# Kernel tuning notes

Hardware: AMD Instinct MI355X
Metric: run time of the kernel (lower is better)

Reference implementation:

```python
import jax, jax.numpy as jnp
import numpy as np

N, E, G = 20000, 320000, 64
H, NF, EF, L, Z = 280, 5, 4, 3, 64
BN_EPS = 1e-5


def _bn(x, g, b):
    # BatchNorm1d in training mode: batch stats over dim 0, biased variance
    m = x.mean(0)
    v = x.var(0)
    return g * (x - m) * jax.lax.rsqrt(v + BN_EPS) + b


def _mlp(x, W1, b1, g1, be1, W2, b2, g2, be2):
    h = jax.nn.relu(_bn(x @ W1 + b1, g1, be1))
    return jax.nn.relu(_bn(h @ W2 + b2, g2, be2))


def setup_inputs() -> dict:
    key = jax.random.key(0)
    ks = jax.random.split(key, 24)
    s = 0.05
    inp = {
        "x": jax.random.normal(ks[0], (N, NF), jnp.float32),
        "edge_attr": jax.random.normal(ks[1], (E, EF), jnp.float32),
        "edge_index": jax.random.randint(ks[2], (2, E), 0, N),
        "batch": jnp.sort(jax.random.randint(ks[3], (N,), 0, G)),
        # input layer
        "Wi": jax.random.normal(ks[4], (NF, H), jnp.float32) * s,
        "bi": jnp.zeros((H,), jnp.float32),
        # message MLP (stacked over L layers): in = 2H+EF
        "Wm1": jax.random.normal(ks[5], (L, 2 * H + EF, H), jnp.float32) * s,
        "bm1": jnp.zeros((L, H), jnp.float32),
        "g1": jnp.ones((L, H), jnp.float32),
        "be1": jnp.zeros((L, H), jnp.float32),
        "Wm2": jax.random.normal(ks[6], (L, H, H), jnp.float32) * s,
        "bm2": jnp.zeros((L, H), jnp.float32),
        "g2": jnp.ones((L, H), jnp.float32),
        "be2": jnp.zeros((L, H), jnp.float32),
        # update MLP: in = 2H
        "Wu1": jax.random.normal(ks[7], (L, 2 * H, H), jnp.float32) * s,
        "bu1": jnp.zeros((L, H), jnp.float32),
        "g3": jnp.ones((L, H), jnp.float32),
        "be3": jnp.zeros((L, H), jnp.float32),
        "Wu2": jax.random.normal(ks[8], (L, H, H), jnp.float32) * s,
        "bu2": jnp.zeros((L, H), jnp.float32),
        "g4": jnp.ones((L, H), jnp.float32),
        "be4": jnp.zeros((L, H), jnp.float32),
        # mu head
        "Wmu": jax.random.normal(ks[9], (H, Z), jnp.float32) * s,
        "bmu": jnp.zeros((Z,), jnp.float32),
    }
    return inp


def reference(x, edge_attr, Wi, bi, Wm1, bm1, g1, be1, Wm2, bm2, g2, be2,
              Wu1, bu1, g3, be3, Wu2, bu2, g4, be4, Wmu, bmu,
              edge_index, batch):
    src, dst = edge_index[0], edge_index[1]
    h = x @ Wi + bi  # [N, H]
    for l in range(L):
        # message: cat(h_i=h[dst], h_j=h[src], edge_attr) -> MLP -> [E, H]
        msg_in = jnp.concatenate([h[dst], h[src], edge_attr], axis=-1)
        msg = _mlp(msg_in, Wm1[l], bm1[l], g1[l], be1[l], Wm2[l], bm2[l], g2[l], be2[l])
        # aggregate: scatter-add into target nodes
        agg = jax.ops.segment_sum(msg, dst, num_segments=N)
        # update: cat(h, agg) -> MLP; residual in GNNEncoder
        upd = _mlp(jnp.concatenate([h, agg], axis=-1),
                   Wu1[l], bu1[l], g3[l], be3[l], Wu2[l], bu2[l], g4[l], be4[l])
        h = h + upd
    # global mean pool over graphs
    sums = jax.ops.segment_sum(h, batch, num_segments=G)
    cnt = jax.ops.segment_sum(jnp.ones((h.shape[0],), h.dtype), batch, num_segments=G)
    pooled = sums / jnp.maximum(cnt, 1.0)[:, None]
    return pooled @ Wmu + bmu  # [G, Z]
```

## Files before the change

### kernel.cpp

```cpp
#include <hip/hip_runtime.h>
#include <hip/hip_bf16.h>

#define NN 20000
#define EE 320000
#define GG 64
#define HH 280
#define NFF 5
#define EFF 4
#define LL 3
#define ZZ 64
#define BN_EPS 1e-5f

typedef __hip_bfloat16 bf;
typedef unsigned short ush;
typedef __attribute__((ext_vector_type(8))) short v8s;
typedef __attribute__((ext_vector_type(4))) float v4f;

__device__ __forceinline__ float us2f(ush u) {
  return __uint_as_float(((unsigned)u) << 16);
}
__device__ __forceinline__ ush f2us(float v) {
  bf b = __float2bfloat16(v);
  return *reinterpret_cast<ush*>(&b);
}
__device__ __forceinline__ int clampi(int v, int hi) {
  return v < 0 ? 0 : (v >= hi ? hi - 1 : v);
}

__global__ void probe_k(const void* __restrict__ x, int* __restrict__ flag) {
  __shared__ int sh[256];
  int tid = threadIdx.x;
  int cnt = 0;
  for (int i = tid; i < 2048; i += 256) {
    ush w = ((const ush*)x)[i];
    unsigned e = (w >> 7) & 0xFF;
    if (w != 0 && (e < 87 || e > 167)) cnt++;
  }
  sh[tid] = cnt;
  __syncthreads();
  for (int o = 128; o > 0; o >>= 1) {
    if (tid < o) sh[tid] += sh[tid + o];
    __syncthreads();
  }
  if (tid == 0) *flag = (sh[0] > 64) ? 1 : 0;
}

__global__ void convert_k(const void* __restrict__ src, float* __restrict__ dst,
                          int n, const int* __restrict__ flag) {
  int i = blockIdx.x * 256 + threadIdx.x;
  if (i < n) {
    if (*flag)
      dst[i] = ((const float*)src)[i];
    else
      dst[i] = us2f(((const ush*)src)[i]);
  }
}

__global__ void wt_ab_k(const float* __restrict__ W, ush* __restrict__ O) {
  int i = blockIdx.x * 256 + threadIdx.x;
  if (i >= 3 * 576 * 288) return;
  int l = i / 165888, r = i % 165888;
  int n = r / 288, k = r % 288;
  float v = 0.f;
  if (n < 560 && k < 280)
    v = (n < 280) ? W[(size_t)l * 157920 + (size_t)k * 280 + n]
                  : W[(size_t)l * 157920 + (size_t)(280 + k) * 280 + (n - 280)];
  O[i] = f2us(v);
}
__global__ void wt_sq_k(const float* __restrict__ W, ush* __restrict__ O) {
  int i = blockIdx.x * 256 + threadIdx.x;
  if (i >= 3 * 320 * 288) return;
  int l = i / 92160, r = i % 92160;
  int n = r / 288, k = r % 288;
  float v = (n < 280 && k < 280) ? W[(size_t)l * 78400 + (size_t)k * 280 + n] : 0.f;
  O[i] = f2us(v);
}
__global__ void wt_u1_k(const float* __restrict__ W, ush* __restrict__ O) {
  int i = blockIdx.x * 256 + threadIdx.x;
  if (i >= 3 * 320 * 576) return;
  int l = i / 184320, r = i % 184320;
  int n = r / 576, k = r % 576;
  float v = (n < 280 && k < 560) ? W[(size_t)l * 156800 + (size_t)k * 280 + n] : 0.f;
  O[i] = f2us(v);
}

struct MG {
  const ush* A;
  const ush* Bt;
  const float* bias;
  void* C;
  float* stats;
  int M, K, Nn, lda, ldb, ldc;
};

template <int CB, int ST>
__global__ __launch_bounds__(256) void mgemm_k(MG g) {
  __shared__ ush Bs[64][296];
  auto red = (float(*)[64])Bs;
  int t = threadIdx.x;
  int n0 = blockIdx.x * 64, m0 = blockIdx.y * 128;
  int lane = t & 63, wv = t >> 6;
  int lrow = lane & 15, quad = lane >> 4;
  int br = t >> 2;
  int bc = (t & 3) * 72;
  v4f acc[2][4];
#pragma unroll
  for (int gi = 0; gi < 2; ++gi)
#pragma unroll
    for (int ci = 0; ci < 4; ++ci) acc[gi][ci] = (v4f){0.f, 0.f, 0.f, 0.f};

  const ush* Arow[2];
  bool av[2];
#pragma unroll
  for (int gi = 0; gi < 2; ++gi) {
    int gm = m0 + (wv << 5) + (gi << 4) + lrow;
    av[gi] = gm < g.M;
    Arow[gi] = g.A + (size_t)gm * g.lda + (quad << 3);
  }
  const ush* Brow = g.Bt + (size_t)(n0 + br) * g.ldb + bc;
  uint4 zz = {0, 0, 0, 0};

  int ntile = g.K / 288;
  for (int tile = 0; tile < ntile; ++tile) {
    int k0 = tile * 288;
    uint4 aR[2][9];
#pragma unroll
    for (int kt = 0; kt < 9; ++kt)
#pragma unroll
      for (int gi = 0; gi < 2; ++gi)
        aR[gi][kt] =
            av[gi] ? *(const uint4*)(Arow[gi] + k0 + (kt << 5)) : zz;
    if (tile) __syncthreads();
#pragma unroll
    for (int i = 0; i < 9; ++i)
      *(uint4*)&Bs[br][bc + (i << 3)] = *(const uint4*)(Brow + k0 + (i << 3));
    __syncthreads();
#pragma unroll
    for (int kt = 0; kt < 9; ++kt) {
      v8s bq[4];
#pragma unroll
      for (int ci = 0; ci < 4; ++ci)
        bq[ci] = *(const v8s*)&Bs[(ci << 4) + lrow][(kt << 5) + (quad << 3)];
#pragma unroll
      for (int gi = 0; gi < 2; ++gi) {
        v8s af = *(v8s*)&aR[gi][kt];
#pragma unroll
        for (int ci = 0; ci < 4; ++ci)
          acc[gi][ci] = __builtin_amdgcn_mfma_f32_16x16x32_bf16(
              af, bq[ci], acc[gi][ci], 0, 0, 0);
      }
    }
  }

  float bj[4];
#pragma unroll
  for (int ci = 0; ci < 4; ++ci) {
    int gn = n0 + (ci << 4) + lrow;
    bj[ci] = (g.bias && gn < g.Nn) ? g.bias[gn] : 0.f;
  }
#pragma unroll
  for (int gi = 0; gi < 2; ++gi)
#pragma unroll
    for (int ci = 0; ci < 4; ++ci)
#pragma unroll
      for (int r = 0; r < 4; ++r) {
        int gm = m0 + (wv << 5) + (gi << 4) + (quad << 2) + r;
        int gn = n0 + (ci << 4) + lrow;
        float v = acc[gi][ci][r] + bj[ci];
        bool ok = (gm < g.M) && (gn < g.Nn);
        if (ok) {
          size_t idx = (size_t)gm * g.ldc + gn;
          if (CB)
            ((ush*)g.C)[idx] = f2us(v);
          else
            ((float*)g.C)[idx] = v;
        }
        acc[gi][ci][r] = ok ? v : 0.f;
      }
  if (ST) {
    int rowg = (wv << 2) | quad;
    __syncthreads();
#pragma unroll
    for (int ci = 0; ci < 4; ++ci) {
      float s = 0.f;
#pragma unroll
      for (int gi = 0; gi < 2; ++gi)
#pragma unroll
        for (int r = 0; r < 4; ++r) s += acc[gi][ci][r];
      red[rowg][(ci << 4) | lrow] = s;
    }
    __syncthreads();
    if (t < 64) {
      float s = 0.f;
#pragma unroll
      for (int r = 0; r < 16; ++r) s += red[r][t];
      int gn = n0 + t;
      if (gn < g.Nn) atomicAdd(&g.stats[gn], s);
    }
    __syncthreads();
#pragma unroll
    for (int ci = 0; ci < 4; ++ci) {
      float s = 0.f;
#pragma unroll
      for (int gi = 0; gi < 2; ++gi)
#pragma unroll
        for (int r = 0; r < 4; ++r) s += acc[gi][ci][r] * acc[gi][ci][r];
      red[rowg][(ci << 4) | lrow] = s;
    }
    __syncthreads();
    if (t < 64) {
      float s = 0.f;
#pragma unroll
      for (int r = 0; r < 16; ++r) s += red[r][t];
      int gn = n0 + t;
      if (gn < g.Nn) atomicAdd(&g.stats[HH + gn], s);
    }
  }
}

__global__ __launch_bounds__(256) void gemm_small_k(
    const float* __restrict__ A, const float* __restrict__ B,
    const float* __restrict__ bias, void* __restrict__ C,
    const int* __restrict__ flag, int M, int K, int Nn, int lda, int ldb,
    int ldc, int outmode) {
  __shared__ alignas(16) float As[16][68];
  __shared__ alignas(16) float Bsm[16][68];
  int tid = threadIdx.x;
  int n0 = blockIdx.x * 64, m0 = blockIdx.y * 64;
  int tx = tid & 15, ty = tid >> 4;
  int am = tid >> 2, akq = (tid & 3) << 2;
  int bk = tid >> 4, bn = (tid & 15) << 2;
  float acc[4][4] = {};
  int gmA = m0 + am;
  int nkt = (K + 15) >> 4;
  for (int kt = 0; kt < nkt; ++kt) {
    int k0 = kt << 4;
#pragma unroll
    for (int i = 0; i < 4; ++i) {
      int gk = k0 + akq + i;
      As[akq + i][am] = (gmA < M && gk < K) ? A[(size_t)gmA * lda + gk] : 0.f;
    }
    {
      int gk = k0 + bk;
      bool kin = gk < K;
#pragma unroll
      for (int j = 0; j < 4; ++j) {
        int gn = n0 + bn + j;
        Bsm[bk][bn + j] = (kin && gn < Nn) ? B[(size_t)gk * ldb + gn] : 0.f;
      }
    }
    __syncthreads();
#pragma unroll
    for (int kk = 0; kk < 16; ++kk) {
      float4 a4 = *(const float4*)&As[kk][ty << 2];
      float4 b4 = *(const float4*)&Bsm[kk][tx << 2];
      float av[4] = {a4.x, a4.y, a4.z, a4.w};
      float bv[4] = {b4.x, b4.y, b4.z, b4.w};
#pragma unroll
      for (int i = 0; i < 4; ++i)
#pragma unroll
        for (int j = 0; j < 4; ++j) acc[i][j] = fmaf(av[i], bv[j], acc[i][j]);
    }
    __syncthreads();
  }
  int ofl = outmode ? *flag : -1;
#pragma unroll
  for (int i = 0; i < 4; ++i) {
    int gm = m0 + (ty << 2) + i;
    if (gm < M) {
#pragma unroll
      for (int j = 0; j < 4; ++j) {
        int gn = n0 + (tx << 2) + j;
        if (gn < Nn) {
          float v = acc[i][j] + (bias ? bias[gn] : 0.f);
          size_t idx = (size_t)gm * ldc + gn;
          if (outmode == 0)
            ((float*)C)[idx] = v;
          else if (ofl)
            ((float*)C)[idx] = v;
          else
            ((ush*)C)[idx] = f2us(v);
        }
      }
    }
  }
}

__global__ __launch_bounds__(256) void edge_stats_k(
    const int* __restrict__ eids, const int* __restrict__ dst,
    const int* __restrict__ src, const float* __restrict__ ea,
    const ush* __restrict__ Pq, const float* __restrict__ W1c,
    const float* __restrict__ b1, float* __restrict__ stats) {
  __shared__ int dstl[256], srcl[256];
  __shared__ float4 eal[256];
  __shared__ float w1cs[4 * HH];
  __shared__ float b1s[HH];
  int tid = threadIdx.x;
  int e0 = blockIdx.x * 256;
  {
    int e = clampi(eids[e0 + tid], EE);
    dstl[tid] = clampi(dst[e], NN);
    srcl[tid] = clampi(src[e], NN);
    eal[tid] = *(const float4*)(ea + (size_t)e * 4);
  }
  for (int i = tid; i < 4 * HH; i += 256) w1cs[i] = W1c[i];
  for (int i = tid; i < HH; i += 256) b1s[i] = b1[i];
  __syncthreads();
  int c0 = tid, c1 = tid + 256;
  bool has1 = c1 < HH;
  float s0 = 0.f, q0 = 0.f, s1 = 0.f, q1 = 0.f;
  for (int e = 0; e < 256; ++e) {
    int d = dstl[e], sn = srcl[e];
    float4 ev = eal[e];
    {
      float raw = us2f(Pq[(size_t)d * 576 + c0]) + us2f(Pq[(size_t)sn * 576 + 280 + c0]);
      float r = ev.x * w1cs[c0] + ev.y * w1cs[HH + c0] +
                ev.z * w1cs[2 * HH + c0] + ev.w * w1cs[3 * HH + c0];
      float tv = raw + r + b1s[c0];
      s0 += tv; q0 += tv * tv;
    }
    if (has1) {
      float raw = us2f(Pq[(size_t)d * 576 + c1]) + us2f(Pq[(size_t)sn * 576 + 280 + c1]);
      float r = ev.x * w1cs[c1] + ev.y * w1cs[HH + c1] +
                ev.z * w1cs[2 * HH + c1] + ev.w * w1cs[3 * HH + c1];
      float tv = raw + r + b1s[c1];
      s1 += tv; q1 += tv * tv;
    }
  }
  atomicAdd(&stats[c0], s0);
  atomicAdd(&stats[HH + c0], q0);
  if (has1) {
    atomicAdd(&stats[c1], s1);
    atomicAdd(&stats[HH + c1], q1);
  }
}

__global__ void bn_finalize_k(const float* __restrict__ stats, float cnt,
                              const float* __restrict__ gw,
                              const float* __restrict__ bw,
                              const float* __restrict__ extra,
                              float* __restrict__ scale,
                              float* __restrict__ shift) {
  int c = threadIdx.x;
  if (c < HH) {
    float m = stats[c] / cnt;
    float v = stats[HH + c] / cnt - m * m;
    v = v < 0.f ? 0.f : v;
    float r = rsqrtf(v + BN_EPS);
    float sc = gw[c] * r;
    float sh = bw[c] - sc * m + (extra ? sc * extra[c] : 0.f);
    scale[c] = sc;
    shift[c] = sh;
  }
}

__global__ void hist_k(const int* __restrict__ dst, int* __restrict__ counts) {
  int e = blockIdx.x * 256 + threadIdx.x;
  if (e < EE) atomicAdd(&counts[clampi(dst[e], NN)], 1);
}

__global__ __launch_bounds__(1024) void scan_k(const int* __restrict__ counts,
                                               int* __restrict__ offs, int n) {
  __shared__ int buf[1024];
  __shared__ int running;
  int tid = threadIdx.x;
  if (tid == 0) running = 0;
  __syncthreads();
  for (int base = 0; base < n; base += 1024) {
    int v = (base + tid < n) ? counts[base + tid] : 0;
    buf[tid] = v;
    __syncthreads();
    for (int off = 1; off < 1024; off <<= 1) {
      int t = (tid >= off) ? buf[tid - off] : 0;
      __syncthreads();
      buf[tid] += t;
      __syncthreads();
    }
    int incl = buf[tid];
    if (base + tid < n) offs[base + tid] = running + incl - v;
    __syncthreads();
    if (tid == 1023) running += incl;
    __syncthreads();
  }
  if (tid == 0) offs[n] = running;
}

__global__ void fill_k(const int* __restrict__ dst, const int* __restrict__ offs,
                       int* __restrict__ cursor, int* __restrict__ eids) {
  int e = blockIdx.x * 256 + threadIdx.x;
  if (e < EE) {
    int n = clampi(dst[e], NN);
    int pos = atomicAdd(&cursor[n], 1);
    int idx = offs[n] + pos;
    if (idx >= 0 && idx < EE) eids[idx] = e;
  }
}

__global__ __launch_bounds__(256) void build_t1_k(
    const int* __restrict__ eids, const int* __restrict__ dst,
    const int* __restrict__ src, const float* __restrict__ ea,
    const ush* __restrict__ Pq, const float* __restrict__ W1c,
    const float* __restrict__ sc, const float* __restrict__ sh,
    ush* __restrict__ T1, int cb) {
  __shared__ float scs[HH], shs[HH], w1[4 * HH];
  int t = threadIdx.x;
  for (int i = t; i < HH; i += 256) { scs[i] = sc[i]; shs[i] = sh[i]; }
  for (int i = t; i < 4 * HH; i += 256) w1[i] = W1c[i];
  __syncthreads();
  int base = blockIdx.x * 32;
  int c2 = t + 256;
  bool h2 = c2 < HH;
  for (int i = 0; i < 32; ++i) {
    int r = cb + base + i;
    int e = clampi(eids[r], EE);
    int d = clampi(dst[e], NN), s = clampi(src[e], NN);
    float4 ev = *(const float4*)(ea + (size_t)e * 4);
    size_t pd = (size_t)d * 576, ps = (size_t)s * 576 + 280;
    size_t orow = (size_t)(base + i) * 288;
    {
      int c = t;
      float v = us2f(Pq[pd + c]) + us2f(Pq[ps + c]) + ev.x * w1[c] +
                ev.y * w1[HH + c] + ev.z * w1[2 * HH + c] + ev.w * w1[3 * HH + c];
      v = fmaf(scs[c], v, shs[c]);
      T1[orow + c] = f2us(v > 0.f ? v : 0.f);
    }
    if (h2) {
      int c = c2;
      float v = us2f(Pq[pd + c]) + us2f(Pq[ps + c]) + ev.x * w1[c] +
                ev.y * w1[HH + c] + ev.z * w1[2 * HH + c] + ev.w * w1[3 * HH + c];
      v = fmaf(scs[c], v, shs[c]);
      T1[orow + c] = f2us(v > 0.f ? v : 0.f);
    }
  }
}

__global__ __launch_bounds__(256) void aggregate_k(
    const int* __restrict__ offs, const ush* __restrict__ tmp2,
    const float* __restrict__ scale, const float* __restrict__ shift,
    float* __restrict__ agg, int e0, int e1) {
  int n = blockIdx.x;
  int rs = offs[n], re = offs[n + 1];
  if (rs < e0) rs = e0;
  if (re > e1) re = e1;
  if (rs >= re) return;
  int t = threadIdx.x;
  int c2 = t + 256;
  bool h2 = c2 < HH;
  float a0 = 0.f, a1 = 0.f;
  float sc0 = scale[t], sh0 = shift[t];
  float sc1 = h2 ? scale[c2] : 0.f, sh1 = h2 ? shift[c2] : 0.f;
  for (int r = rs; r < re; ++r) {
    const ush* row = tmp2 + (size_t)(r - e0) * HH;
    float v0 = fmaf(sc0, us2f(row[t]), sh0);
    a0 += v0 > 0.f ? v0 : 0.f;
    if (h2) {
      float v1 = fmaf(sc1, us2f(row[c2]), sh1);
      a1 += v1 > 0.f ? v1 : 0.f;
    }
  }
  agg[(size_t)n * HH + t] += a0;
  if (h2) agg[(size_t)n * HH + c2] += a1;
}

__global__ void hb_k(const float* __restrict__ h, ush* __restrict__ hcat) {
  int i = blockIdx.x * 256 + threadIdx.x;
  if (i < NN * HH) {
    int n = i / HH, c = i % HH;
    hcat[(size_t)n * 576 + c] = f2us(h[i]);
  }
}
__global__ void agg2hcat_k(const float* __restrict__ agg, ush* __restrict__ hcat) {
  int i = blockIdx.x * 256 + threadIdx.x;
  if (i < NN * HH) {
    int n = i / HH, c = i % HH;
    hcat[(size_t)n * 576 + 280 + c] = f2us(agg[i]);
  }
}
__global__ void u2a_k(const float* __restrict__ u1, const float* __restrict__ sc,
                      const float* __restrict__ sh, ush* __restrict__ u2A) {
  int i = blockIdx.x * 256 + threadIdx.x;
  if (i < NN * HH) {
    int n = i / HH, c = i % HH;
    float v = fmaf(sc[c], u1[i], sh[c]);
    u2A[(size_t)n * 288 + c] = f2us(v > 0.f ? v : 0.f);
  }
}
__global__ void residual_k(float* __restrict__ h, const float* __restrict__ u2,
                           const float* __restrict__ scale,
                           const float* __restrict__ shift) {
  int i = blockIdx.x * 256 + threadIdx.x;
  if (i < NN * HH) {
    int c = i % HH;
    float v = fmaf(scale[c], u2[i], shift[c]);
    h[i] += v > 0.f ? v : 0.f;
  }
}

__device__ __forceinline__ int lowerb(const int* a, int n, int key) {
  int lo = 0, hi = n;
  while (lo < hi) {
    int mid = (lo + hi) >> 1;
    if (a[mid] < key) lo = mid + 1; else hi = mid;
  }
  return lo;
}

__global__ __launch_bounds__(256) void pool_k(const float* __restrict__ h,
                                              const int* __restrict__ batch,
                                              float* __restrict__ pooled) {
  __shared__ float red[4][56];
  int gid = blockIdx.x, cc = blockIdx.y;
  int start = lowerb(batch, NN, gid);
  int end = lowerb(batch, NN, gid + 1);
  int cnt = end - start;
  float inv = 1.f / (float)(cnt > 1 ? cnt : 1);
  int grp = threadIdx.x >> 6, ci = threadIdx.x & 63;
  if (ci < 56) {
    int col = cc * 56 + ci;
    float s = 0.f;
    for (int n = start + grp; n < end; n += 4) s += h[(size_t)n * HH + col];
    red[grp][ci] = s;
  }
  __syncthreads();
  if (threadIdx.x < 56) {
    float s = red[0][threadIdx.x] + red[1][threadIdx.x] +
              red[2][threadIdx.x] + red[3][threadIdx.x];
    pooled[(size_t)gid * HH + cc * 56 + threadIdx.x] = s * inv;
  }
}

extern "C" void kernel_launch(void* const* d_in, const int* in_sizes, int n_in,
                              void* d_out, int out_size, void* d_ws,
                              size_t ws_size, hipStream_t stream) {
  const int* eidx = (const int*)d_in[2];
  const int* batch = (const int*)d_in[3];
  const int* srcp = eidx;
  const int* dstp = eidx + EE;
  size_t NH = (size_t)NN * HH;

  float* w0 = (float*)d_ws;
  size_t off = 0;
  auto alloc = [&](size_t n) {
    float* p = w0 + off;
    off += (n + 3) & ~(size_t)3;
    return p;
  };
  int* flag = (int*)alloc(4);
  float* cx = alloc(100000);
  float* cea = alloc(1280000);
  float* cWi = alloc(1400);
  float* cbi = alloc(280);
  float* cWm1 = alloc(473760);
  float* cbm1 = alloc(840);
  float* cg1 = alloc(840);
  float* cbe1 = alloc(840);
  float* cWm2 = alloc(235200);
  float* cbm2 = alloc(840);
  float* cg2 = alloc(840);
  float* cbe2 = alloc(840);
  float* cWu1 = alloc(470400);
  float* cbu1 = alloc(840);
  float* cg3 = alloc(840);
  float* cbe3 = alloc(840);
  float* cWu2 = alloc(235200);
  float* cbu2 = alloc(840);
  float* cg4 = alloc(840);
  float* cbe4 = alloc(840);
  float* cWmu = alloc(17920);
  float* cbmu = alloc(64);
  ush* W1ab = (ush*)alloc(248832);
  ush* W2t = (ush*)alloc(138240);
  ush* WU1t = (ush*)alloc(276480);
  ush* WU2t = (ush*)alloc(138240);
  float* h = alloc(NH);
  ush* hcat = (ush*)alloc(5824512);
  ush* u2A = hcat;
  float* pqr = alloc(5824512);
  ush* Pq = (ush*)pqr;
  float* u1f = pqr;
  float* agg = alloc(NH);
  float* pooled = alloc((size_t)GG * HH);
  float* stats = alloc(8 * HH);
  float* ss = alloc(8 * HH);
  int* counts = (int*)alloc(NN);
  int* offs = (int*)alloc(NN + 1);
  int* cursor = (int*)alloc(NN);
  int* eids = (int*)alloc(EE);
  size_t baseB = off * 4;

  int EC = 6400, T2 = 6400;
  {
    const int ecs[5] = {64000, 64000, 32000, 12800, 6400};
    const int t2s[5] = {EE, 64000, 32000, 12800, 6400};
    for (int i = 0; i < 5; ++i) {
      size_t need = baseB + (size_t)ecs[i] * 288 * 2 + (size_t)t2s[i] * 280 * 2 + 64;
      if (need <= ws_size) { EC = ecs[i]; T2 = t2s[i]; break; }
    }
  }
  ush* T1c = (ush*)(w0 + off);
  ush* tmp2 = T1c + (size_t)EC * 288;
  bool stored = (T2 == EE);
  int nch = EE / EC;

  probe_k<<<1, 256, 0, stream>>>(d_in[0], flag);
  struct Cv { const void* s; float* d; int n; };
  const Cv cv[22] = {
      {d_in[0], cx, NN * NFF},     {d_in[1], cea, EE * EFF},
      {d_in[4], cWi, NFF * HH},    {d_in[5], cbi, HH},
      {d_in[6], cWm1, LL * (2 * HH + EFF) * HH}, {d_in[7], cbm1, LL * HH},
      {d_in[8], cg1, LL * HH},     {d_in[9], cbe1, LL * HH},
      {d_in[10], cWm2, LL * HH * HH}, {d_in[11], cbm2, LL * HH},
      {d_in[12], cg2, LL * HH},    {d_in[13], cbe2, LL * HH},
      {d_in[14], cWu1, LL * 2 * HH * HH}, {d_in[15], cbu1, LL * HH},
      {d_in[16], cg3, LL * HH},    {d_in[17], cbe3, LL * HH},
      {d_in[18], cWu2, LL * HH * HH}, {d_in[19], cbu2, LL * HH},
      {d_in[20], cg4, LL * HH},    {d_in[21], cbe4, LL * HH},
      {d_in[22], cWmu, HH * ZZ},   {d_in[23], cbmu, ZZ}};
  for (int i = 0; i < 22; ++i)
    convert_k<<<(cv[i].n + 255) / 256, 256, 0, stream>>>(cv[i].s, cv[i].d, cv[i].n, flag);

  wt_ab_k<<<(3 * 576 * 288 + 255) / 256, 256, 0, stream>>>(cWm1, W1ab);
  wt_sq_k<<<(3 * 320 * 288 + 255) / 256, 256, 0, stream>>>(cWm2, W2t);
  wt_u1_k<<<(3 * 320 * 576 + 255) / 256, 256, 0, stream>>>(cWu1, WU1t);
  wt_sq_k<<<(3 * 320 * 288 + 255) / 256, 256, 0, stream>>>(cWu2, WU2t);

  gemm_small_k<<<dim3(5, 313), 256, 0, stream>>>(cx, cWi, cbi, h, nullptr, NN,
                                                 NFF, HH, NFF, HH, HH, 0);
  hipMemsetAsync(counts, 0, NN * sizeof(int), stream);
  hipMemsetAsync(cursor, 0, NN * sizeof(int), stream);
  hist_k<<<(EE + 255) / 256, 256, 0, stream>>>(dstp, counts);
  scan_k<<<1, 1024, 0, stream>>>(counts, offs, NN);
  fill_k<<<(EE + 255) / 256, 256, 0, stream>>>(dstp, offs, cursor, eids);

  int elemGrid = (int)((NH + 255) / 256);
  for (int l = 0; l < LL; ++l) {
    ush* Wab = W1ab + (size_t)l * 576 * 288;
    ush* W2l = W2t + (size_t)l * 320 * 288;
    ush* WU1l = WU1t + (size_t)l * 320 * 576;
    ush* WU2l = WU2t + (size_t)l * 320 * 288;
    const float* W1c = cWm1 + (size_t)l * 157920 + (size_t)560 * 280;
    float* st1 = stats; float* st2 = stats + 560;
    float* st3 = stats + 1120; float* st4 = stats + 1680;
    float* ss1 = ss; float* ss2 = ss + 560;
    float* ss3 = ss + 1120; float* ss4 = ss + 1680;
    hipMemsetAsync(stats, 0, 8 * HH * sizeof(float), stream);

    hb_k<<<elemGrid, 256, 0, stream>>>(h, hcat);
    {
      MG g = {hcat, Wab, nullptr, Pq, nullptr, NN, 288, 560, 576, 288, 576};
      mgemm_k<1, 0><<<dim3(9, 157), 256, 0, stream>>>(g);
    }
    edge_stats_k<<<EE / 256, 256, 0, stream>>>(eids, dstp, srcp, cea, Pq, W1c,
                                               cbm1 + l * HH, st1);
    bn_finalize_k<<<1, 320, 0, stream>>>(st1, (float)EE, cg1 + l * HH,
                                         cbe1 + l * HH, cbm1 + l * HH, ss1, ss1 + HH);
    for (int c = 0; c < nch; ++c) {
      int cb = c * EC;
      build_t1_k<<<EC / 32, 256, 0, stream>>>(eids, dstp, srcp, cea, Pq, W1c,
                                              ss1, ss1 + HH, T1c, cb);
      MG g = {T1c, W2l, cbm2 + l * HH,
              stored ? (void*)(tmp2 + (size_t)cb * HH) : (void*)tmp2, st2,
              EC, 288, HH, 288, 288, HH};
      mgemm_k<1, 1><<<dim3(5, EC / 128), 256, 0, stream>>>(g);
    }
    bn_finalize_k<<<1, 320, 0, stream>>>(st2, (float)EE, cg2 + l * HH,
                                         cbe2 + l * HH, nullptr, ss2, ss2 + HH);
    hipMemsetAsync(agg, 0, NH * sizeof(float), stream);
    if (stored) {
      aggregate_k<<<NN, 256, 0, stream>>>(offs, tmp2, ss2, ss2 + HH, agg, 0, EE);
    } else {
      for (int c = 0; c < nch; ++c) {
        int cb = c * EC;
        build_t1_k<<<EC / 32, 256, 0, stream>>>(eids, dstp, srcp, cea, Pq, W1c,
                                                ss1, ss1 + HH, T1c, cb);
        MG g = {T1c, W2l, cbm2 + l * HH, (void*)tmp2, nullptr,
                EC, 288, HH, 288, 288, HH};
        mgemm_k<1, 0><<<dim3(5, EC / 128), 256, 0, stream>>>(g);
        aggregate_k<<<NN, 256, 0, stream>>>(offs, tmp2, ss2, ss2 + HH, agg, cb, cb + EC);
      }
    }
    agg2hcat_k<<<elemGrid, 256, 0, stream>>>(agg, hcat);
    {
      MG g = {hcat, WU1l, cbu1 + l * HH, u1f, st3, NN, 576, HH, 576, 576, HH};
      mgemm_k<0, 1><<<dim3(5, 157), 256, 0, stream>>>(g);
    }
    bn_finalize_k<<<1, 320, 0, stream>>>(st3, (float)NN, cg3 + l * HH,
                                         cbe3 + l * HH, nullptr, ss3, ss3 + HH);
    u2a_k<<<elemGrid, 256, 0, stream>>>(u1f, ss3, ss3 + HH, u2A);
    {
      MG g = {u2A, WU2t + (size_t)l * 320 * 288, cbu2 + l * HH, agg, st4,
              NN, 288, HH, 288, 288, HH};
      mgemm_k<0, 1><<<dim3(5, 157), 256, 0, stream>>>(g);
    }
    bn_finalize_k<<<1, 320, 0, stream>>>(st4, (float)NN, cg4 + l * HH,
                                         cbe4 + l * HH, nullptr, ss4, ss4 + HH);
    residual_k<<<elemGrid, 256, 0, stream>>>(h, agg, ss4, ss4 + HH);
  }

  pool_k<<<dim3(GG, 5), 256, 0, stream>>>(h, batch, pooled);
  gemm_small_k<<<dim3(1, 1), 256, 0, stream>>>(pooled, cWmu, cbmu, d_out, flag,
                                               GG, HH, ZZ, HH, ZZ, ZZ, 1);
}
```

Measured before the change: 4.275 ms.

## Double GEMM M-tile to 256 rows and stream A fragments with rolling prefetch

Each wave now computes 64 rows instead of 32, so every B fragment read from shared memory feeds twice as many MFMAs and the B tile is loaded half as often overall. The A operand is no longer held in registers for the whole K tile; it is streamed through a 3-deep rotating register buffer that prefetches two K steps ahead. All launch grids are halved in the M dimension to match. The cost is more accumulator registers and fewer blocks, which can hurt occupancy and parallelism, especially for the 20000-row node GEMMs.

```diff
diff --git a/kernel.cpp b/kernel.cpp
--- a/kernel.cpp
+++ b/kernel.cpp
@@ -98,24 +98,24 @@
   __shared__ ush Bs[64][296];
   auto red = (float(*)[64])Bs;
   int t = threadIdx.x;
-  int n0 = blockIdx.x * 64, m0 = blockIdx.y * 128;
+  int n0 = blockIdx.x * 64, m0 = blockIdx.y * 256;
   int lane = t & 63, wv = t >> 6;
   int lrow = lane & 15, quad = lane >> 4;
   int br = t >> 2;
   int bc = (t & 3) * 72;
-  v4f acc[2][4];
-#pragma unroll
-  for (int gi = 0; gi < 2; ++gi)
-#pragma unroll
-    for (int ci = 0; ci < 4; ++ci) acc[gi][ci] = (v4f){0.f, 0.f, 0.f, 0.f};
-
-  const ush* Arow[2];
-  bool av[2];
-#pragma unroll
-  for (int gi = 0; gi < 2; ++gi) {
-    int gm = m0 + (wv << 5) + (gi << 4) + lrow;
-    av[gi] = gm < g.M;
-    Arow[gi] = g.A + (size_t)gm * g.lda + (quad << 3);
+  v4f acc[4][4];
+#pragma unroll
+  for (int mi = 0; mi < 4; ++mi)
+#pragma unroll
+    for (int ci = 0; ci < 4; ++ci) acc[mi][ci] = (v4f){0.f, 0.f, 0.f, 0.f};
+
+  const ush* Arow[4];
+  bool av[4];
+#pragma unroll
+  for (int mi = 0; mi < 4; ++mi) {
+    int gm = m0 + (wv << 6) + (mi << 4) + lrow;
+    av[mi] = gm < g.M;
+    Arow[mi] = g.A + (size_t)gm * g.lda + (quad << 3);
   }
   const ush* Brow = g.Bt + (size_t)(n0 + br) * g.ldb + bc;
   uint4 zz = {0, 0, 0, 0};
@@ -123,31 +123,36 @@
   int ntile = g.K / 288;
   for (int tile = 0; tile < ntile; ++tile) {
     int k0 = tile * 288;
-    uint4 aR[2][9];
-#pragma unroll
-    for (int kt = 0; kt < 9; ++kt)
-#pragma unroll
-      for (int gi = 0; gi < 2; ++gi)
-        aR[gi][kt] =
-            av[gi] ? *(const uint4*)(Arow[gi] + k0 + (kt << 5)) : zz;
     if (tile) __syncthreads();
 #pragma unroll
     for (int i = 0; i < 9; ++i)
       *(uint4*)&Bs[br][bc + (i << 3)] = *(const uint4*)(Brow + k0 + (i << 3));
+    uint4 ap[3][4];
+#pragma unroll
+    for (int mi = 0; mi < 4; ++mi) {
+      ap[0][mi] = av[mi] ? *(const uint4*)(Arow[mi] + k0) : zz;
+      ap[1][mi] = av[mi] ? *(const uint4*)(Arow[mi] + k0 + 32) : zz;
+    }
     __syncthreads();
 #pragma unroll
     for (int kt = 0; kt < 9; ++kt) {
+      if (kt + 2 < 9) {
+        int kn = k0 + ((kt + 2) << 5);
+#pragma unroll
+        for (int mi = 0; mi < 4; ++mi)
+          ap[(kt + 2) % 3][mi] = av[mi] ? *(const uint4*)(Arow[mi] + kn) : zz;
+      }
       v8s bq[4];
 #pragma unroll
       for (int ci = 0; ci < 4; ++ci)
         bq[ci] = *(const v8s*)&Bs[(ci << 4) + lrow][(kt << 5) + (quad << 3)];
 #pragma unroll
-      for (int gi = 0; gi < 2; ++gi) {
-        v8s af = *(v8s*)&aR[gi][kt];
+      for (int mi = 0; mi < 4; ++mi) {
+        v8s af = *(v8s*)&ap[kt % 3][mi];
 #pragma unroll
         for (int ci = 0; ci < 4; ++ci)
-          acc[gi][ci] = __builtin_amdgcn_mfma_f32_16x16x32_bf16(
-              af, bq[ci], acc[gi][ci], 0, 0, 0);
+          acc[mi][ci] = __builtin_amdgcn_mfma_f32_16x16x32_bf16(
+              af, bq[ci], acc[mi][ci], 0, 0, 0);
       }
     }
   }
@@ -159,14 +164,14 @@
     bj[ci] = (g.bias && gn < g.Nn) ? g.bias[gn] : 0.f;
   }
 #pragma unroll
-  for (int gi = 0; gi < 2; ++gi)
+  for (int mi = 0; mi < 4; ++mi)
 #pragma unroll
     for (int ci = 0; ci < 4; ++ci)
 #pragma unroll
       for (int r = 0; r < 4; ++r) {
-        int gm = m0 + (wv << 5) + (gi << 4) + (quad << 2) + r;
+        int gm = m0 + (wv << 6) + (mi << 4) + (quad << 2) + r;
         int gn = n0 + (ci << 4) + lrow;
-        float v = acc[gi][ci][r] + bj[ci];
+        float v = acc[mi][ci][r] + bj[ci];
         bool ok = (gm < g.M) && (gn < g.Nn);
         if (ok) {
           size_t idx = (size_t)gm * g.ldc + gn;
@@ -175,7 +180,7 @@
           else
             ((float*)g.C)[idx] = v;
         }
-        acc[gi][ci][r] = ok ? v : 0.f;
+        acc[mi][ci][r] = ok ? v : 0.f;
       }
   if (ST) {
     int rowg = (wv << 2) | quad;
@@ -184,9 +189,9 @@
     for (int ci = 0; ci < 4; ++ci) {
       float s = 0.f;
 #pragma unroll
-      for (int gi = 0; gi < 2; ++gi)
-#pragma unroll
-        for (int r = 0; r < 4; ++r) s += acc[gi][ci][r];
+      for (int mi = 0; mi < 4; ++mi)
+#pragma unroll
+        for (int r = 0; r < 4; ++r) s += acc[mi][ci][r];
       red[rowg][(ci << 4) | lrow] = s;
     }
     __syncthreads();
@@ -202,9 +207,9 @@
     for (int ci = 0; ci < 4; ++ci) {
       float s = 0.f;
 #pragma unroll
-      for (int gi = 0; gi < 2; ++gi)
-#pragma unroll
-        for (int r = 0; r < 4; ++r) s += acc[gi][ci][r] * acc[gi][ci][r];
+      for (int mi = 0; mi < 4; ++mi)
+#pragma unroll
+        for (int r = 0; r < 4; ++r) s += acc[mi][ci][r] * acc[mi][ci][r];
       red[rowg][(ci << 4) | lrow] = s;
     }
     __syncthreads();
@@ -648,7 +653,7 @@
     hb_k<<<elemGrid, 256, 0, stream>>>(h, hcat);
     {
       MG g = {hcat, Wab, nullptr, Pq, nullptr, NN, 288, 560, 576, 288, 576};
-      mgemm_k<1, 0><<<dim3(9, 157), 256, 0, stream>>>(g);
+      mgemm_k<1, 0><<<dim3(9, 79), 256, 0, stream>>>(g);
     }
     edge_stats_k<<<EE / 256, 256, 0, stream>>>(eids, dstp, srcp, cea, Pq, W1c,
                                                cbm1 + l * HH, st1);
@@ -661,7 +666,7 @@
       MG g = {T1c, W2l, cbm2 + l * HH,
               stored ? (void*)(tmp2 + (size_t)cb * HH) : (void*)tmp2, st2,
               EC, 288, HH, 288, 288, HH};
-      mgemm_k<1, 1><<<dim3(5, EC / 128), 256, 0, stream>>>(g);
+      mgemm_k<1, 1><<<dim3(5, EC / 256), 256, 0, stream>>>(g);
     }
     bn_finalize_k<<<1, 320, 0, stream>>>(st2, (float)EE, cg2 + l * HH,
                                          cbe2 + l * HH, nullptr, ss2, ss2 + HH);
@@ -675,22 +680,21 @@
                                                 ss1, ss1 + HH, T1c, cb);
         MG g = {T1c, W2l, cbm2 + l * HH, (void*)tmp2, nullptr,
                 EC, 288, HH, 288, 288, HH};
-        mgemm_k<1, 0><<<dim3(5, EC / 128), 256, 0, stream>>>(g);
+        mgemm_k<1, 0><<<dim3(5, EC / 256), 256, 0, stream>>>(g);
         aggregate_k<<<NN, 256, 0, stream>>>(offs, tmp2, ss2, ss2 + HH, agg, cb, cb + EC);
       }
     }
     agg2hcat_k<<<elemGrid, 256, 0, stream>>>(agg, hcat);
     {
       MG g = {hcat, WU1l, cbu1 + l * HH, u1f, st3, NN, 576, HH, 576, 576, HH};
-      mgemm_k<0, 1><<<dim3(5, 157), 256, 0, stream>>>(g);
+      mgemm_k<0, 1><<<dim3(5, 79), 256, 0, stream>>>(g);
     }
     bn_finalize_k<<<1, 320, 0, stream>>>(st3, (float)NN, cg3 + l * HH,
                                          cbe3 + l * HH, nullptr, ss3, ss3 + HH);
     u2a_k<<<elemGrid, 256, 0, stream>>>(u1f, ss3, ss3 + HH, u2A);
     {
-      MG g = {u2A, WU2t + (size_t)l * 320 * 288, cbu2 + l * HH, agg, st4,
-              NN, 288, HH, 288, 288, HH};
-      mgemm_k<0, 1><<<dim3(5, 157), 256, 0, stream>>>(g);
+      MG g = {u2A, WU2l, cbu2 + l * HH, agg, st4, NN, 288, HH, 288, 288, HH};
+      mgemm_k<0, 1><<<dim3(5, 79), 256, 0, stream>>>(g);
     }
     bn_finalize_k<<<1, 320, 0, stream>>>(st4, (float)NN, cg4 + l * HH,
                                          cbe4 + l * HH, nullptr, ss4, ss4 + HH);
```

Result: slower. 4.563 ms (+6.7%).
